# Kernel optimization log

Hardware: AMD Instinct MI355X
Metric: run time of the kernel (lower is better)

The kernel has to match this reference:

```python
import jax, jax.numpy as jnp
import numpy as np

NUM_HEADS = 16
ROPE_BASE = 10000.0


def _rope_cos_sin(seq_len, head_dim, dtype):
    inv_freq = 1.0 / (ROPE_BASE ** (jnp.arange(0, head_dim, 2, dtype=jnp.float32) / head_dim))
    freqs = jnp.arange(seq_len, dtype=jnp.float32)[:, None] * inv_freq[None, :]  # [L, hd/2]
    return jnp.cos(freqs).astype(dtype), jnp.sin(freqs).astype(dtype)


def _apply_rope(t, cos, sin):
    # t: [B, H, L, hd]; cos/sin: [L, hd/2] broadcast over B,H
    x1 = t[..., ::2]
    x2 = t[..., 1::2]
    r1 = x1 * cos - x2 * sin
    r2 = x1 * sin + x2 * cos
    return jnp.stack([r1, r2], axis=-1).reshape(t.shape)


def setup_inputs() -> dict:
    key = jax.random.key(0)
    k1, k2, k3 = jax.random.split(key, 3)
    B, L, D = 2, 2048, 1024
    x = jax.random.normal(k1, (B, L, D), dtype=jnp.float32)
    W_qkv = jax.random.normal(k2, (3 * D, D), dtype=jnp.float32) * (D ** -0.5)
    W_out = jax.random.normal(k3, (D, D), dtype=jnp.float32) * (D ** -0.5)
    return {"x": x, "W_qkv": W_qkv, "W_out": W_out}


def reference(x, W_qkv, W_out):
    B, L, D = x.shape
    H = NUM_HEADS
    hd = D // H
    scale = hd ** -0.5

    qkv = x @ W_qkv.T                              # [B, L, 3D]
    qkv = qkv.reshape(B, L, 3, H, hd)
    qkv = jnp.transpose(qkv, (2, 0, 3, 1, 4))      # [3, B, H, L, hd]
    q, k, v = qkv[0], qkv[1], qkv[2]

    cos, sin = _rope_cos_sin(L, hd, x.dtype)
    q = _apply_rope(q, cos, sin)
    k = _apply_rope(k, cos, sin)

    logits = jnp.einsum("bhqd,bhkd->bhqk", q, k) * scale
    attn = jax.nn.softmax(logits, axis=-1)         # dropout p=0.0 -> identity
    out = jnp.einsum("bhqk,bhkd->bhqd", attn, v)   # [B, H, L, hd]
    out = jnp.transpose(out, (0, 2, 1, 3)).reshape(B, L, D)
    return out @ W_out.T
```

## Files before the change

### kernel.cpp

```cpp
#include <hip/hip_runtime.h>
#include <hip/hip_bf16.h>
#include <stdint.h>


typedef __bf16 bf16x8 __attribute__((ext_vector_type(8)));
typedef float f32x4 __attribute__((ext_vector_type(4)));

__device__ __forceinline__ unsigned short f2bf(float f) {
  union { float f; unsigned int u; } v; v.f = f;
  unsigned int r = v.u + 0x7FFFu + ((v.u >> 16) & 1u);
  return (unsigned short)(r >> 16);
}
__device__ __forceinline__ float b2f(unsigned short u) {
  union { unsigned int u; float f; } v; v.u = ((unsigned int)u) << 16;
  return v.f;
}

__device__ __forceinline__ void gl2lds16(const void* gptr, void* lptr) {
  __builtin_amdgcn_global_load_lds(
      (const __attribute__((address_space(1))) unsigned int*)gptr,
      (__attribute__((address_space(3))) unsigned int*)lptr, 16, 0, 0);
}

__global__ void cvt_bf16(const float4* __restrict__ in, ushort4* __restrict__ out, int n4) {
  int i = blockIdx.x * 256 + threadIdx.x;
  if (i >= n4) return;
  float4 v = in[i];
  ushort4 o;
  o.x = f2bf(v.x); o.y = f2bf(v.y); o.z = f2bf(v.z); o.w = f2bf(v.w);
  out[i] = o;
}

template<int OUT_BF16>
__global__ __launch_bounds__(256) void gemm_bt(
    const __hip_bfloat16* __restrict__ A,
    const __hip_bfloat16* __restrict__ B,
    void* __restrict__ C, int M, int N, int K) {
  __shared__ __align__(16) __hip_bfloat16 As[128 * 32];
  __shared__ __align__(16) __hip_bfloat16 Bs[128 * 32];
  const int tid = threadIdx.x;
  const int lane = tid & 63;
  const int wave = tid >> 6;
  const int wm = (wave >> 1) * 64, wn = (wave & 1) * 64;
  const int g = lane >> 4, lr = lane & 15;
  const int m0 = blockIdx.y * 128, n0 = blockIdx.x * 128;
  f32x4 acc[4][4] = {};

  const char* Ag = (const char*)(A + (size_t)m0 * K);
  const char* Bg = (const char*)(B + (size_t)n0 * K);
  const size_t ldb = (size_t)K * 2;

  for (int kt = 0; kt < K; kt += 32) {
    const char* Ak = Ag + (size_t)kt * 2;
    const char* Bk = Bg + (size_t)kt * 2;
#pragma unroll
    for (int j = 0; j < 2; ++j) {
      int c = tid + j * 256;
      int row = c >> 2;
      int colb = (c & 3) * 16;
      gl2lds16(Ak + (size_t)row * ldb + colb, (char*)As + c * 16);
      gl2lds16(Bk + (size_t)row * ldb + colb, (char*)Bs + c * 16);
    }
    asm volatile("s_waitcnt vmcnt(0)" ::: "memory");
    __syncthreads();
    bf16x8 af[4], bfr[4];
#pragma unroll
    for (int i = 0; i < 4; ++i)
      af[i] = *(const bf16x8*)((const char*)As + (size_t)(wm + i * 16 + lr) * 64 + g * 16);
#pragma unroll
    for (int i = 0; i < 4; ++i)
      bfr[i] = *(const bf16x8*)((const char*)Bs + (size_t)(wn + i * 16 + lr) * 64 + g * 16);
#pragma unroll
    for (int i = 0; i < 4; ++i)
#pragma unroll
      for (int j = 0; j < 4; ++j)
        acc[i][j] = __builtin_amdgcn_mfma_f32_16x16x32_bf16(af[i], bfr[j], acc[i][j], 0, 0, 0);
    __syncthreads();
  }

#pragma unroll
  for (int i = 0; i < 4; ++i) {
#pragma unroll
    for (int j = 0; j < 4; ++j) {
      int n = n0 + wn + j * 16 + lr;
#pragma unroll
      for (int r = 0; r < 4; ++r) {
        int m = m0 + wm + i * 16 + g * 4 + r;
        float v = acc[i][j][r];
        if (OUT_BF16) {
          ((unsigned short*)C)[(size_t)m * N + n] = f2bf(v);
        } else {
          ((float*)C)[(size_t)m * N + n] = v;
        }
      }
    }
  }
}

__global__ void rope_scatter(const __hip_bfloat16* __restrict__ qkv,
                             __hip_bfloat16* __restrict__ Qs,
                             __hip_bfloat16* __restrict__ Ks,
                             __hip_bfloat16* __restrict__ Vt) {
  const int t = blockIdx.x * 256 + threadIdx.x;
  const int i = t & 31;
  const int lc = (t >> 5) & 255;
  const int h = (t >> 13) & 15;
  const int b = t >> 17;
  const float inv_freq = powf(10000.0f, -(float)i * (1.0f / 32.0f));
  const unsigned short* qk = (const unsigned short*)qkv;
  unsigned short v0[8], v1[8];
#pragma unroll
  for (int j = 0; j < 8; ++j) {
    const int l = lc * 8 + j;
    const size_t row = ((size_t)(b * 2048 + l)) * 3072;
    float s, c;
    sincosf((float)l * inv_freq, &s, &c);
    ushort2 qp = *(const ushort2*)(qk + row + h * 64 + 2 * i);
    ushort2 kp = *(const ushort2*)(qk + row + 1024 + h * 64 + 2 * i);
    ushort2 vp = *(const ushort2*)(qk + row + 2048 + h * 64 + 2 * i);
    float x1 = b2f(qp.x), x2 = b2f(qp.y);
    float y1 = b2f(kp.x), y2 = b2f(kp.y);
    size_t oidx = (((size_t)(b * 16 + h)) * 2048 + l) * 64 + 2 * i;
    ushort2 qo, ko;
    qo.x = f2bf((x1 * c - x2 * s) * 0.125f);
    qo.y = f2bf((x1 * s + x2 * c) * 0.125f);
    ko.x = f2bf(y1 * c - y2 * s);
    ko.y = f2bf(y1 * s + y2 * c);
    *(ushort2*)((unsigned short*)Qs + oidx) = qo;
    *(ushort2*)((unsigned short*)Ks + oidx) = ko;
    v0[j] = vp.x; v1[j] = vp.y;
  }
  unsigned short* Vtu = (unsigned short*)Vt;
  const size_t vrow0 = (((size_t)(b * 16 + h)) * 64 + 2 * i) * 2048 + lc * 8;
  const size_t vrow1 = vrow0 + 2048;
  *(ushort4*)(Vtu + vrow0)     = make_ushort4(v0[0], v0[1], v0[2], v0[3]);
  *(ushort4*)(Vtu + vrow0 + 4) = make_ushort4(v0[4], v0[5], v0[6], v0[7]);
  *(ushort4*)(Vtu + vrow1)     = make_ushort4(v1[0], v1[1], v1[2], v1[3]);
  *(ushort4*)(Vtu + vrow1 + 4) = make_ushort4(v1[4], v1[5], v1[6], v1[7]);
}

__global__ __launch_bounds__(256) void attn_fwd(
    const __hip_bfloat16* __restrict__ Qs,
    const __hip_bfloat16* __restrict__ Ks,
    const __hip_bfloat16* __restrict__ Vt,
    __hip_bfloat16* __restrict__ Ob) {
  constexpr int L = 2048;
  __shared__ __align__(16) __hip_bfloat16 Kt[64 * 64];
  __shared__ __align__(16) __hip_bfloat16 Vts[64 * 64];
  __shared__ __align__(16) __hip_bfloat16 Pw[4][16][72];
  const int tid = threadIdx.x, lane = tid & 63, w = tid >> 6;
  const int g = lane >> 4, lr = lane & 15;
  const int bh = blockIdx.x >> 5;
  const int qt = blockIdx.x & 31;
  const int q = qt * 64 + w * 16 + lr;

  const __hip_bfloat16* Qrow = Qs + ((size_t)bh * L + q) * 64;
  bf16x8 qf[2];
  qf[0] = *(const bf16x8*)(Qrow + g * 8);
  qf[1] = *(const bf16x8*)(Qrow + 32 + g * 8);

  f32x4 oacc[4] = {};
  float mrun = -1e30f, lpart = 0.0f;
  const char* Kbase = (const char*)(Ks + (size_t)bh * L * 64);
  const char* Vbase = (const char*)(Vt + (size_t)bh * 64 * L);

  for (int kt = 0; kt < L / 64; ++kt) {
#pragma unroll
    for (int j = 0; j < 2; ++j) {
      int c = tid + j * 256;
      int o = c * 16;
      int os = o ^ (((o >> 7) & 7) << 4);
      gl2lds16(Kbase + (size_t)kt * 8192 + os, (char*)Kt + o);
      int vrow = os >> 7, vcol = os & 127;
      gl2lds16(Vbase + (size_t)vrow * (L * 2) + kt * 128 + vcol, (char*)Vts + o);
    }
    asm volatile("s_waitcnt vmcnt(0)" ::: "memory");
    __syncthreads();

    f32x4 sacc[4] = {};
#pragma unroll
    for (int mf = 0; mf < 4; ++mf) {
      int row = mf * 16 + lr;
#pragma unroll
      for (int ds = 0; ds < 2; ++ds) {
        int addr = (row * 128 + ds * 64 + g * 16) ^ ((row & 7) << 4);
        bf16x8 a = *(const bf16x8*)((const char*)Kt + addr);
        sacc[mf] = __builtin_amdgcn_mfma_f32_16x16x32_bf16(a, qf[ds], sacc[mf], 0, 0, 0);
      }
    }

    float tmax = -1e30f;
#pragma unroll
    for (int mf = 0; mf < 4; ++mf)
#pragma unroll
      for (int r = 0; r < 4; ++r) tmax = fmaxf(tmax, sacc[mf][r]);
    tmax = fmaxf(tmax, __shfl_xor(tmax, 16));
    tmax = fmaxf(tmax, __shfl_xor(tmax, 32));
    float mnew = fmaxf(mrun, tmax);
    float alpha = __expf(mrun - mnew);
    mrun = mnew;
    lpart *= alpha;
#pragma unroll
    for (int d = 0; d < 4; ++d) oacc[d] = oacc[d] * alpha;
#pragma unroll
    for (int mf = 0; mf < 4; ++mf) {
      float p0 = __expf(sacc[mf][0] - mnew);
      float p1 = __expf(sacc[mf][1] - mnew);
      float p2 = __expf(sacc[mf][2] - mnew);
      float p3 = __expf(sacc[mf][3] - mnew);
      lpart += (p0 + p1) + (p2 + p3);
      ushort4 pk;
      pk.x = f2bf(p0); pk.y = f2bf(p1); pk.z = f2bf(p2); pk.w = f2bf(p3);
      *(ushort4*)((char*)(&Pw[w][lr][0]) + mf * 32 + g * 8) = pk;
    }
    asm volatile("s_waitcnt lgkmcnt(0)" ::: "memory");
    __builtin_amdgcn_sched_barrier(0);

#pragma unroll
    for (int ks = 0; ks < 2; ++ks) {
      bf16x8 pfrag = *(const bf16x8*)((const char*)(&Pw[w][lr][0]) + ks * 64 + g * 16);
#pragma unroll
      for (int df = 0; df < 4; ++df) {
        int row = df * 16 + lr;
        int addr = (row * 128 + ks * 64 + g * 16) ^ ((row & 7) << 4);
        bf16x8 a = *(const bf16x8*)((const char*)Vts + addr);
        oacc[df] = __builtin_amdgcn_mfma_f32_16x16x32_bf16(a, pfrag, oacc[df], 0, 0, 0);
      }
    }
    __syncthreads();
  }

  float lsum = lpart;
  lsum += __shfl_xor(lsum, 16);
  lsum += __shfl_xor(lsum, 32);
  float inv = 1.0f / lsum;

  const int b = bh >> 4, h = bh & 15;
  unsigned short* orow = (unsigned short*)Ob + ((size_t)(b * L + q)) * 1024 + h * 64;
#pragma unroll
  for (int df = 0; df < 4; ++df) {
    ushort4 o4;
    o4.x = f2bf(oacc[df][0] * inv);
    o4.y = f2bf(oacc[df][1] * inv);
    o4.z = f2bf(oacc[df][2] * inv);
    o4.w = f2bf(oacc[df][3] * inv);
    *(ushort4*)(orow + df * 16 + g * 4) = o4;
  }
}

extern "C" void kernel_launch(void* const* d_in, const int* in_sizes, int n_in,
                              void* d_out, int out_size, void* d_ws, size_t ws_size,
                              hipStream_t stream) {
  (void)in_sizes; (void)n_in; (void)out_size; (void)ws_size;
  const float* x    = (const float*)d_in[0];
  const float* wqkv = (const float*)d_in[1];
  const float* wout = (const float*)d_in[2];

  char* ws = (char*)d_ws;
  auto* xb   = (__hip_bfloat16*)(ws + (size_t)(0u));
  auto* wqb  = (__hip_bfloat16*)(ws + ((size_t)8u << 20));
  auto* wob  = (__hip_bfloat16*)(ws + ((size_t)14u << 20));
  auto* qkvb = (__hip_bfloat16*)(ws + ((size_t)16u << 20));
  auto* Ob   = (__hip_bfloat16*)(ws + ((size_t)16u << 20));
  auto* Qsb  = (__hip_bfloat16*)(ws + ((size_t)40u << 20));
  auto* Ksb  = (__hip_bfloat16*)(ws + ((size_t)48u << 20));
  auto* Vtb  = (__hip_bfloat16*)(ws + ((size_t)56u << 20));

  cvt_bf16<<<4096, 256, 0, stream>>>((const float4*)x,    (ushort4*)xb,  1048576);
  cvt_bf16<<<3072, 256, 0, stream>>>((const float4*)wqkv, (ushort4*)wqb, 786432);
  cvt_bf16<<<1024, 256, 0, stream>>>((const float4*)wout, (ushort4*)wob, 262144);

  gemm_bt<1><<<dim3(24, 32), 256, 0, stream>>>(xb, wqb, (void*)qkvb, 4096, 3072, 1024);
  rope_scatter<<<1024, 256, 0, stream>>>(qkvb, Qsb, Ksb, Vtb);
  attn_fwd<<<1024, 256, 0, stream>>>(Qsb, Ksb, Vtb, Ob);
  gemm_bt<0><<<dim3(8, 32), 256, 0, stream>>>(Ob, wob, d_out, 4096, 1024, 1024);
}
```

Before: 160.5 us.

## Double-buffer attention K/V tiles, use exp2 softmax with lazy rescale, fuse conversions

The attention kernel now double-buffers K/V tiles in LDS, so the next tile's global-to-LDS load overlaps compute on the current one. Softmax switches to exp2 by folding log2(e) into the Q scale, and it only rescales the accumulator when the running max grows by more than 8. Block indices are remapped so neighbouring blocks cover different heads. The three fp32-to-bf16 conversion launches become one kernel. The extra LDS buffer may reduce occupancy, and the lazy rescale allows exponentials up to 2^8 before normalisation, which slightly changes bf16 rounding of P.

```diff
diff --git a/kernel.cpp b/kernel.cpp
--- a/kernel.cpp
+++ b/kernel.cpp
@@ -4,6 +4,7 @@
 
 
 typedef __bf16 bf16x8 __attribute__((ext_vector_type(8)));
+typedef __bf16 bf16x4v __attribute__((ext_vector_type(4)));
 typedef float f32x4 __attribute__((ext_vector_type(4)));
 
 __device__ __forceinline__ unsigned short f2bf(float f) {
@@ -22,13 +23,18 @@
       (__attribute__((address_space(3))) unsigned int*)lptr, 16, 0, 0);
 }
 
-__global__ void cvt_bf16(const float4* __restrict__ in, ushort4* __restrict__ out, int n4) {
+__global__ void cvt_all(const float4* __restrict__ x,
+                        const float4* __restrict__ wq,
+                        const float4* __restrict__ wo,
+                        ushort4* __restrict__ dst) {
   int i = blockIdx.x * 256 + threadIdx.x;
-  if (i >= n4) return;
-  float4 v = in[i];
+  float4 v;
+  if (i < 1048576) v = x[i];
+  else if (i < 1835008) v = wq[i - 1048576];
+  else v = wo[i - 1835008];
   ushort4 o;
   o.x = f2bf(v.x); o.y = f2bf(v.y); o.z = f2bf(v.z); o.w = f2bf(v.w);
-  out[i] = o;
+  dst[i] = o;
 }
 
 template<int OUT_BF16>
@@ -107,6 +113,7 @@
   const int h = (t >> 13) & 15;
   const int b = t >> 17;
   const float inv_freq = powf(10000.0f, -(float)i * (1.0f / 32.0f));
+  const float QSCALE = 0.125f * 1.44269504088896f;
   const unsigned short* qk = (const unsigned short*)qkv;
   unsigned short v0[8], v1[8];
 #pragma unroll
@@ -122,8 +129,8 @@
     float y1 = b2f(kp.x), y2 = b2f(kp.y);
     size_t oidx = (((size_t)(b * 16 + h)) * 2048 + l) * 64 + 2 * i;
     ushort2 qo, ko;
-    qo.x = f2bf((x1 * c - x2 * s) * 0.125f);
-    qo.y = f2bf((x1 * s + x2 * c) * 0.125f);
+    qo.x = f2bf((x1 * c - x2 * s) * QSCALE);
+    qo.y = f2bf((x1 * s + x2 * c) * QSCALE);
     ko.x = f2bf(y1 * c - y2 * s);
     ko.y = f2bf(y1 * s + y2 * c);
     *(ushort2*)((unsigned short*)Qs + oidx) = qo;
@@ -145,13 +152,16 @@
     const __hip_bfloat16* __restrict__ Vt,
     __hip_bfloat16* __restrict__ Ob) {
   constexpr int L = 2048;
-  __shared__ __align__(16) __hip_bfloat16 Kt[64 * 64];
-  __shared__ __align__(16) __hip_bfloat16 Vts[64 * 64];
+  constexpr int NT = L / 64;
+  __shared__ __align__(16) __hip_bfloat16 Kt[2][64 * 64];
+  __shared__ __align__(16) __hip_bfloat16 Vts[2][64 * 64];
   __shared__ __align__(16) __hip_bfloat16 Pw[4][16][72];
   const int tid = threadIdx.x, lane = tid & 63, w = tid >> 6;
   const int g = lane >> 4, lr = lane & 15;
-  const int bh = blockIdx.x >> 5;
-  const int qt = blockIdx.x & 31;
+  const int blk = blockIdx.x;
+  const int slot = blk >> 3;
+  const int bh = (blk & 7) * 4 + (slot >> 5);
+  const int qt = slot & 31;
   const int q = qt * 64 + w * 16 + lr;
 
   const __hip_bfloat16* Qrow = Qs + ((size_t)bh * L + q) * 64;
@@ -164,18 +174,32 @@
   const char* Kbase = (const char*)(Ks + (size_t)bh * L * 64);
   const char* Vbase = (const char*)(Vt + (size_t)bh * 64 * L);
 
-  for (int kt = 0; kt < L / 64; ++kt) {
+  auto stage = [&](int buf, int kt) {
 #pragma unroll
     for (int j = 0; j < 2; ++j) {
       int c = tid + j * 256;
       int o = c * 16;
       int os = o ^ (((o >> 7) & 7) << 4);
-      gl2lds16(Kbase + (size_t)kt * 8192 + os, (char*)Kt + o);
+      gl2lds16(Kbase + (size_t)kt * 8192 + os, (char*)Kt[buf] + o);
       int vrow = os >> 7, vcol = os & 127;
-      gl2lds16(Vbase + (size_t)vrow * (L * 2) + kt * 128 + vcol, (char*)Vts + o);
-    }
-    asm volatile("s_waitcnt vmcnt(0)" ::: "memory");
-    __syncthreads();
+      gl2lds16(Vbase + (size_t)vrow * (L * 2) + kt * 128 + vcol, (char*)Vts[buf] + o);
+    }
+  };
+
+  stage(0, 0);
+
+  for (int kt = 0; kt < NT; ++kt) {
+    const int cur = kt & 1;
+    if (kt + 1 < NT) {
+      stage(cur ^ 1, kt + 1);
+      asm volatile("s_waitcnt vmcnt(4)" ::: "memory");
+    } else {
+      asm volatile("s_waitcnt vmcnt(0)" ::: "memory");
+    }
+    __builtin_amdgcn_s_barrier();
+
+    const char* Kc = (const char*)Kt[cur];
+    const char* Vc = (const char*)Vts[cur];
 
     f32x4 sacc[4] = {};
 #pragma unroll
@@ -184,34 +208,35 @@
 #pragma unroll
       for (int ds = 0; ds < 2; ++ds) {
         int addr = (row * 128 + ds * 64 + g * 16) ^ ((row & 7) << 4);
-        bf16x8 a = *(const bf16x8*)((const char*)Kt + addr);
+        bf16x8 a = *(const bf16x8*)(Kc + addr);
         sacc[mf] = __builtin_amdgcn_mfma_f32_16x16x32_bf16(a, qf[ds], sacc[mf], 0, 0, 0);
       }
     }
 
-    float tmax = -1e30f;
-#pragma unroll
-    for (int mf = 0; mf < 4; ++mf)
-#pragma unroll
-      for (int r = 0; r < 4; ++r) tmax = fmaxf(tmax, sacc[mf][r]);
+    float t0 = fmaxf(fmaxf(sacc[0][0], sacc[0][1]), fmaxf(sacc[0][2], sacc[0][3]));
+    float t1 = fmaxf(fmaxf(sacc[1][0], sacc[1][1]), fmaxf(sacc[1][2], sacc[1][3]));
+    float t2 = fmaxf(fmaxf(sacc[2][0], sacc[2][1]), fmaxf(sacc[2][2], sacc[2][3]));
+    float t3 = fmaxf(fmaxf(sacc[3][0], sacc[3][1]), fmaxf(sacc[3][2], sacc[3][3]));
+    float tmax = fmaxf(fmaxf(t0, t1), fmaxf(t2, t3));
     tmax = fmaxf(tmax, __shfl_xor(tmax, 16));
     tmax = fmaxf(tmax, __shfl_xor(tmax, 32));
-    float mnew = fmaxf(mrun, tmax);
-    float alpha = __expf(mrun - mnew);
-    mrun = mnew;
-    lpart *= alpha;
-#pragma unroll
-    for (int d = 0; d < 4; ++d) oacc[d] = oacc[d] * alpha;
+    if (__any(tmax > mrun + 8.0f)) {
+      float mnew = fmaxf(mrun, tmax);
+      float alpha = __builtin_amdgcn_exp2f(mrun - mnew);
+      mrun = mnew;
+      lpart *= alpha;
+#pragma unroll
+      for (int d = 0; d < 4; ++d) oacc[d] = oacc[d] * alpha;
+    }
 #pragma unroll
     for (int mf = 0; mf < 4; ++mf) {
-      float p0 = __expf(sacc[mf][0] - mnew);
-      float p1 = __expf(sacc[mf][1] - mnew);
-      float p2 = __expf(sacc[mf][2] - mnew);
-      float p3 = __expf(sacc[mf][3] - mnew);
+      float p0 = __builtin_amdgcn_exp2f(sacc[mf][0] - mrun);
+      float p1 = __builtin_amdgcn_exp2f(sacc[mf][1] - mrun);
+      float p2 = __builtin_amdgcn_exp2f(sacc[mf][2] - mrun);
+      float p3 = __builtin_amdgcn_exp2f(sacc[mf][3] - mrun);
       lpart += (p0 + p1) + (p2 + p3);
-      ushort4 pk;
-      pk.x = f2bf(p0); pk.y = f2bf(p1); pk.z = f2bf(p2); pk.w = f2bf(p3);
-      *(ushort4*)((char*)(&Pw[w][lr][0]) + mf * 32 + g * 8) = pk;
+      bf16x4v pk = { (__bf16)p0, (__bf16)p1, (__bf16)p2, (__bf16)p3 };
+      *(bf16x4v*)((char*)(&Pw[w][lr][0]) + mf * 32 + g * 8) = pk;
     }
     asm volatile("s_waitcnt lgkmcnt(0)" ::: "memory");
     __builtin_amdgcn_sched_barrier(0);
@@ -223,11 +248,11 @@
       for (int df = 0; df < 4; ++df) {
         int row = df * 16 + lr;
         int addr = (row * 128 + ks * 64 + g * 16) ^ ((row & 7) << 4);
-        bf16x8 a = *(const bf16x8*)((const char*)Vts + addr);
+        bf16x8 a = *(const bf16x8*)(Vc + addr);
         oacc[df] = __builtin_amdgcn_mfma_f32_16x16x32_bf16(a, pfrag, oacc[df], 0, 0, 0);
       }
     }
-    __syncthreads();
+    __builtin_amdgcn_s_barrier();
   }
 
   float lsum = lpart;
@@ -266,9 +291,8 @@
   auto* Ksb  = (__hip_bfloat16*)(ws + ((size_t)48u << 20));
   auto* Vtb  = (__hip_bfloat16*)(ws + ((size_t)56u << 20));
 
-  cvt_bf16<<<4096, 256, 0, stream>>>((const float4*)x,    (ushort4*)xb,  1048576);
-  cvt_bf16<<<3072, 256, 0, stream>>>((const float4*)wqkv, (ushort4*)wqb, 786432);
-  cvt_bf16<<<1024, 256, 0, stream>>>((const float4*)wout, (ushort4*)wob, 262144);
+  cvt_all<<<8192, 256, 0, stream>>>((const float4*)x, (const float4*)wqkv,
+                                    (const float4*)wout, (ushort4*)xb);
 
   gemm_bt<1><<<dim3(24, 32), 256, 0, stream>>>(xb, wqb, (void*)qkvb, 4096, 3072, 1024);
   rope_scatter<<<1024, 256, 0, stream>>>(qkvb, Qsb, Ksb, Vtb);
```

Result: slower. 168.5 us (+5.0%).
